# Performance work log

Hardware: AMD Instinct MI355X
Metric: run time of the kernel (lower is better)

The kernel has to match this reference:

```python
import jax, jax.numpy as jnp
import numpy as np

# Forest layout: 6 levels, children of node i at level L are contiguous at level L+1.
LEVEL_SIZES = [4096, 16384, 65536, 131072, 262144, 262144]
OFF = np.concatenate([[0], np.cumsum(LEVEL_SIZES)]).astype(np.int64)
N_NODES = int(OFF[-1])
VOCAB = 50000
D_IN = 128
HID = 128
N_CLASS = 4
W_SCALE = 0.08  # keep gate pre-activations in a sane range


def setup_inputs() -> dict:
    key = jax.random.key(0)
    ks = jax.random.split(key, 24)
    inp = {}
    inp["sen"] = jax.random.randint(ks[0], (N_NODES,), 0, VOCAB, dtype=jnp.int32)
    inp["embedding"] = jax.random.normal(ks[1], (VOCAB, D_IN), jnp.float32)
    names = ["ix", "ih", "fx", "fh", "ox", "oh", "ux", "uh"]
    for j, nm in enumerate(names):
        din = D_IN if nm.endswith("x") else HID
        inp["W_" + nm] = jax.random.normal(ks[2 + j], (din, HID), jnp.float32) * W_SCALE
        inp["b_" + nm] = jnp.zeros((HID,), jnp.float32)
    inp["W_out"] = jax.random.normal(ks[20], (HID, N_CLASS), jnp.float32) * W_SCALE
    inp["b_out"] = jnp.zeros((N_CLASS,), jnp.float32)
    return inp


def _forward(sen, embedding, W_ix, b_ix, W_ih, b_ih, W_fx, b_fx, W_fh, b_fh,
             W_ox, b_ox, W_oh, b_oh, W_ux, b_ux, W_uh, b_uh, W_out, b_out):
    emb = embedding[sen]                               # [N, D_in] gather
    h_all = jnp.zeros((N_NODES, HID), emb.dtype)
    c_all = jnp.zeros((N_NODES, HID), emb.dtype)
    L_last = len(LEVEL_SIZES) - 1
    for L in range(L_last, -1, -1):                    # bottom-up over levels
        o0, o1 = int(OFF[L]), int(OFF[L + 1])
        nL = LEVEL_SIZES[L]
        x = emb[o0:o1]                                 # [nL, D_in]
        if L == L_last:                                # leaves: no children
            h_sum = jnp.zeros((nL, HID), emb.dtype)
            fc_sum = jnp.zeros((nL, HID), emb.dtype)
        else:
            c0, c1 = int(OFF[L + 1]), int(OFF[L + 2])
            ratio = LEVEL_SIZES[L + 1] // nL           # children per node
            hc = h_all[c0:c1].reshape(nL, ratio, HID)  # children h
            cc = c_all[c0:c1].reshape(nL, ratio, HID)  # children c
            h_sum = hc.sum(axis=1)
            # per-child forget gate: sigmoid(fx(x_parent) + fh(h_child))
            f = jax.nn.sigmoid((x @ W_fx + b_fx)[:, None, :] + hc @ W_fh + b_fh)
            fc_sum = (f * cc).sum(axis=1)
        i = jax.nn.sigmoid(x @ W_ix + b_ix + h_sum @ W_ih + b_ih)
        og = jax.nn.sigmoid(x @ W_ox + b_ox + h_sum @ W_oh + b_oh)
        u = jnp.tanh(x @ W_ux + b_ux + h_sum @ W_uh + b_uh)
        c = i * u + fc_sum
        h = og * jnp.tanh(c)
        h_all = h_all.at[o0:o1].set(h)
        c_all = c_all.at[o0:o1].set(c)
    root_h = h_all[: LEVEL_SIZES[0]]                   # level-0 nodes
    return root_h @ W_out + b_out                      # [n_roots, 4] logits


def reference(sen, embedding, W_ix, b_ix, W_ih, b_ih, W_fx, b_fx, W_fh, b_fh,
              W_ox, b_ox, W_oh, b_oh, W_ux, b_ux, W_uh, b_uh, W_out, b_out):
    return _forward(sen, embedding, W_ix, b_ix, W_ih, b_ih, W_fx, b_fx, W_fh, b_fh,
                    W_ox, b_ox, W_oh, b_oh, W_ux, b_ux, W_uh, b_uh, W_out, b_out)
```

## Files before the change

### kernel.cpp

```cpp
#include <hip/hip_runtime.h>
#include <hip/hip_bf16.h>
#include <cstdio>

typedef unsigned short u16;
typedef __bf16 bf16x8 __attribute__((ext_vector_type(8)));
typedef float  floatx4 __attribute__((ext_vector_type(4)));

__device__ __forceinline__ float bf2f(u16 u) {
  union { unsigned int i; float f; } v; v.i = ((unsigned int)u) << 16; return v.f;
}
__device__ __forceinline__ u16 f2bf(float f) {
  union { float f; unsigned int i; } v; v.f = f;
  unsigned int x = v.i;
  return (u16)((x + 0x7fffu + ((x >> 16) & 1u)) >> 16);
}
__device__ __forceinline__ unsigned int f2bf_pk(float a, float b) {
  __hip_bfloat162 h = __float22bfloat162_rn(make_float2(a, b));
  union { __hip_bfloat162 h; unsigned int u; } v; v.h = h; return v.u;
}
__device__ __forceinline__ float sigmoidf_(float x) {
  return __builtin_amdgcn_rcpf(1.f + __expf(-x));
}
__device__ __forceinline__ float tanhf_(float x) {
  return fmaf(-2.f, __builtin_amdgcn_rcpf(1.f + __expf(2.f * x)), 1.f);
}

__device__ __forceinline__ int swz128(int row, int c16) {
  return row * 128 + ((c16 ^ (row & 15)) << 3);
}
__device__ __forceinline__ int swze(int row, int col) {
  return row * 128 + (((((col >> 3)) ^ (row & 15)) << 3) | (col & 7));
}

__global__ __launch_bounds__(256, 2) void proj_e(
    const float* __restrict__ emb, const u16* __restrict__ WT,
    const float* __restrict__ bsum, u16* __restrict__ Ep)
{
  __shared__ __align__(16) u16 ldsA[128 * 128];
  const int tid = threadIdx.x;
  const long m0 = (long)blockIdx.x * 128;
  {
    const int r = tid >> 1, half = tid & 1;
    long row = m0 + r; if (row > 49999) row = 49999;
    const float* src = emb + row * 128 + half * 64;
#pragma unroll
    for (int i = 0; i < 8; i++) {
      float4 v0 = *reinterpret_cast<const float4*>(src + i * 8);
      float4 v1 = *reinterpret_cast<const float4*>(src + i * 8 + 4);
      unsigned int ov[4] = { f2bf_pk(v0.x, v0.y), f2bf_pk(v0.z, v0.w),
                             f2bf_pk(v1.x, v1.y), f2bf_pk(v1.z, v1.w) };
      *reinterpret_cast<uint4*>(&ldsA[swz128(r, half * 8 + i)]) =
          *reinterpret_cast<const uint4*>(ov);
    }
  }
  __syncthreads();
  const int lane = tid & 63, w = tid >> 6, l16 = lane & 15, quad = lane >> 4;
#pragma unroll
  for (int half = 0; half < 2; half++) {
    const int col = w * 32 + half * 16 + l16;
    bf16x8 bI[4], bU[4], bO[4], bF[4];
#pragma unroll
    for (int ks = 0; ks < 4; ks++) {
      const size_t o_ = ks * 32 + quad * 8;
      bI[ks] = *reinterpret_cast<const bf16x8*>(WT + (size_t)(0   + col) * 128 + o_);
      bU[ks] = *reinterpret_cast<const bf16x8*>(WT + (size_t)(128 + col) * 128 + o_);
      bO[ks] = *reinterpret_cast<const bf16x8*>(WT + (size_t)(256 + col) * 128 + o_);
      bF[ks] = *reinterpret_cast<const bf16x8*>(WT + (size_t)(384 + col) * 128 + o_);
    }
    const float bi = bsum[col], bu = bsum[128 + col], bo = bsum[256 + col], bf = bsum[384 + col];
#pragma unroll
    for (int i = 0; i < 8; i++) {
      floatx4 aI = {0.f,0.f,0.f,0.f}, aU = {0.f,0.f,0.f,0.f};
      floatx4 aO = {0.f,0.f,0.f,0.f}, aF = {0.f,0.f,0.f,0.f};
#pragma unroll
      for (int ks = 0; ks < 4; ks++) {
        bf16x8 a = *reinterpret_cast<const bf16x8*>(&ldsA[swz128(i * 16 + l16, ks * 4 + quad)]);
        aI = __builtin_amdgcn_mfma_f32_16x16x32_bf16(a, bI[ks], aI, 0, 0, 0);
        aU = __builtin_amdgcn_mfma_f32_16x16x32_bf16(a, bU[ks], aU, 0, 0, 0);
        aO = __builtin_amdgcn_mfma_f32_16x16x32_bf16(a, bO[ks], aO, 0, 0, 0);
        aF = __builtin_amdgcn_mfma_f32_16x16x32_bf16(a, bF[ks], aF, 0, 0, 0);
      }
#pragma unroll
      for (int r2 = 0; r2 < 4; r2++) {
        const long row = m0 + i * 16 + quad * 4 + r2;
        if (row < 50000) {
          u16 ov[4] = { f2bf(aI[r2] + bi), f2bf(aU[r2] + bu),
                        f2bf(aO[r2] + bo), f2bf(aF[r2] + bf) };
          *reinterpret_cast<ushort4*>(Ep + row * 512 + col * 4) =
              *reinterpret_cast<const ushort4*>(ov);
        }
      }
    }
  }
}

__global__ void leaf_hc(const u16* __restrict__ Ep,
                        u16* __restrict__ Hl, u16* __restrict__ Cl)
{
  const int tid = threadIdx.x;
  const int r = tid >> 6, c2 = tid & 63;
  const size_t v = (size_t)blockIdx.x * 4 + r;
  uint4 g = *reinterpret_cast<const uint4*>(Ep + v * 512 + (size_t)c2 * 8);
  const u16* p = reinterpret_cast<const u16*>(&g);
  float c0 = sigmoidf_(bf2f(p[0])) * tanhf_(bf2f(p[1]));
  float c1 = sigmoidf_(bf2f(p[4])) * tanhf_(bf2f(p[5]));
  float h0 = sigmoidf_(bf2f(p[2])) * tanhf_(c0);
  float h1 = sigmoidf_(bf2f(p[6])) * tanhf_(c1);
  *reinterpret_cast<unsigned int*>(Hl + v * 128 + c2 * 2) = f2bf_pk(h0, h1);
  *reinterpret_cast<unsigned int*>(Cl + v * 128 + c2 * 2) = f2bf_pk(c0, c1);
}

__global__ __launch_bounds__(256, 2) void k_l3fused(
    const int* __restrict__ sen, const u16* __restrict__ Ep,
    const u16* __restrict__ Hl, const u16* __restrict__ Cl,
    const u16* __restrict__ BfT, const u16* __restrict__ BihT,
    const u16* __restrict__ BuhT, const u16* __restrict__ BohT,
    u16* __restrict__ c_out, u16* __restrict__ h_out,
    long o0, long o1, long o2)
{
  constexpr int PM = 32, CM = 64, NCI = 4, RT = 2;
  __shared__ __align__(16) u16 ldsH[CM * 128];
  __shared__ __align__(16) u16 ldsC[CM * 128];
  __shared__ __align__(16) u16 ldsA[CM * 128];
  __shared__ int sidC[CM];
  __shared__ int sidP[PM];

  const int tid = threadIdx.x;
  const long p0 = (long)blockIdx.x * PM;
  const long cb = (long)blockIdx.x * CM;

  {
    const int r = (tid & 127) >> 1, half = tid & 1;
    const size_t vc = (size_t)sen[o2 + cb + r];
    if (tid < 128) {
      const u16* hs = Hl + vc * 128;
#pragma unroll
      for (int ii = 0; ii < 8; ii++) {
        const int c16 = half * 8 + ii;
        *reinterpret_cast<uint4*>(&ldsH[swz128(r, c16)]) =
            *reinterpret_cast<const uint4*>(hs + c16 * 8);
      }
    } else {
      const u16* cs = Cl + vc * 128;
#pragma unroll
      for (int ii = 0; ii < 8; ii++) {
        const int c16 = half * 8 + ii;
        *reinterpret_cast<uint4*>(&ldsC[swz128(r, c16)]) =
            *reinterpret_cast<const uint4*>(cs + c16 * 8);
      }
    }
    if (tid < CM) sidC[tid] = sen[o1 + cb + tid];
    if (tid < PM) sidP[tid] = sen[o0 + p0 + tid];
  }
  __syncthreads();

  const int lane = tid & 63, w = tid >> 6, l16 = lane & 15, quad = lane >> 4;

#define LDE(I,R2) (*reinterpret_cast<const ushort4*>( \
    Ep + (size_t)sidC[(I) * 16 + quad * 4 + (R2)] * 512 + col * 4))
#define EPI1(R2, E) { \
    const int row = rbase + (R2); \
    const float iv = sigmoidf_(aI[R2] + bf2f((E).x)); \
    const float uv = tanhf_   (aU[R2] + bf2f((E).y)); \
    const float ov = sigmoidf_(aO[R2] + bf2f((E).z)); \
    const float fv = sigmoidf_(aF[R2] + bf2f((E).w)); \
    const int sl = swze(row, col); \
    const float c4 = fmaf(iv, uv, fv * bf2f(ldsC[sl])); \
    const float h4 = ov * tanhf_(c4); \
    ldsC[sl] = f2bf(c4); \
    ldsA[sl] = f2bf(h4); \
  }
#pragma unroll
  for (int gl = 0; gl < 2; gl++) {
    const int col = w * 32 + gl * 16 + l16;
    ushort4 e0 = LDE(0, 0), e1 = LDE(0, 1), e2 = LDE(0, 2), e3 = LDE(0, 3);
    bf16x8 hI[4], hU[4], hO[4], hF[4];
#pragma unroll
    for (int ks = 0; ks < 4; ks++) {
      const size_t ho = (size_t)col * 128 + ks * 32 + quad * 8;
      hI[ks] = *reinterpret_cast<const bf16x8*>(BihT + ho);
      hU[ks] = *reinterpret_cast<const bf16x8*>(BuhT + ho);
      hO[ks] = *reinterpret_cast<const bf16x8*>(BohT + ho);
      hF[ks] = *reinterpret_cast<const bf16x8*>(BfT  + ho);
    }
#pragma unroll
    for (int i = 0; i < NCI; i++) {
      ushort4 n0 = e0, n1 = e1, n2 = e2, n3 = e3;
      if (i + 1 < NCI) {
        n0 = LDE(i + 1, 0); n1 = LDE(i + 1, 1);
        n2 = LDE(i + 1, 2); n3 = LDE(i + 1, 3);
      }
      floatx4 aI = {0.f,0.f,0.f,0.f}, aU = {0.f,0.f,0.f,0.f};
      floatx4 aO = {0.f,0.f,0.f,0.f}, aF = {0.f,0.f,0.f,0.f};
#pragma unroll
      for (int ks = 0; ks < 4; ks++) {
        bf16x8 ah = *reinterpret_cast<const bf16x8*>(&ldsH[swz128(i * 16 + l16, ks * 4 + quad)]);
        aI = __builtin_amdgcn_mfma_f32_16x16x32_bf16(ah, hI[ks], aI, 0, 0, 0);
        aU = __builtin_amdgcn_mfma_f32_16x16x32_bf16(ah, hU[ks], aU, 0, 0, 0);
        aO = __builtin_amdgcn_mfma_f32_16x16x32_bf16(ah, hO[ks], aO, 0, 0, 0);
        aF = __builtin_amdgcn_mfma_f32_16x16x32_bf16(ah, hF[ks], aF, 0, 0, 0);
      }
      const int rbase = i * 16 + quad * 4;
      EPI1(0, e0) EPI1(1, e1) EPI1(2, e2) EPI1(3, e3)
      e0 = n0; e1 = n1; e2 = n2; e3 = n3;
    }
  }
#undef LDE
#undef EPI1
  __syncthreads();

#define LDG(I,T) (*reinterpret_cast<const ushort4*>( \
    Ep + (size_t)sidP[(((I) * 16 + quad * 4) >> 1) + (T)] * 512 + col * 4))
#define EPI2(T, G) { \
    const int p = (rbase >> 1) + (T); \
    const float epf = bf2f((G).w); \
    float fsum = 0.f, isum = 0.f, usum = 0.f, osum = 0.f; \
    _Pragma("unroll") \
    for (int r2 = (T) * RT; r2 < (T) * RT + RT; r2++) { \
      const int row = rbase + r2; \
      const float cch = bf2f(ldsC[swze(row, col)]); \
      fsum += sigmoidf_(aF[r2] + epf) * cch; \
      isum += aI[r2]; usum += aU[r2]; osum += aO[r2]; \
    } \
    const float c = sigmoidf_(isum + bf2f((G).x)) * tanhf_(usum + bf2f((G).y)) + fsum; \
    const float h = sigmoidf_(osum + bf2f((G).z)) * tanhf_(c); \
    c_out[(p0 + p) * 128 + col] = f2bf(c); \
    h_out[(p0 + p) * 128 + col] = f2bf(h); \
  }
#pragma unroll
  for (int gl = 0; gl < 2; gl++) {
    const int col = w * 32 + gl * 16 + l16;
    ushort4 g0 = LDG(0, 0), g1 = LDG(0, 1);
    bf16x8 bF[4], bI[4], bU[4], bO[4];
#pragma unroll
    for (int ks = 0; ks < 4; ks++) {
      const size_t bo_ = (size_t)col * 128 + ks * 32 + quad * 8;
      bF[ks] = *reinterpret_cast<const bf16x8*>(BfT + bo_);
      bI[ks] = *reinterpret_cast<const bf16x8*>(BihT + bo_);
      bU[ks] = *reinterpret_cast<const bf16x8*>(BuhT + bo_);
      bO[ks] = *reinterpret_cast<const bf16x8*>(BohT + bo_);
    }
#pragma unroll
    for (int i = 0; i < NCI; i++) {
      ushort4 m0 = g0, m1 = g1;
      if (i + 1 < NCI) { m0 = LDG(i + 1, 0); m1 = LDG(i + 1, 1); }
      floatx4 aF = {0.f,0.f,0.f,0.f}, aI = {0.f,0.f,0.f,0.f};
      floatx4 aU = {0.f,0.f,0.f,0.f}, aO = {0.f,0.f,0.f,0.f};
#pragma unroll
      for (int ks = 0; ks < 4; ks++) {
        bf16x8 a = *reinterpret_cast<const bf16x8*>(&ldsA[swz128(i * 16 + l16, ks * 4 + quad)]);
        aF = __builtin_amdgcn_mfma_f32_16x16x32_bf16(a, bF[ks], aF, 0, 0, 0);
        aI = __builtin_amdgcn_mfma_f32_16x16x32_bf16(a, bI[ks], aI, 0, 0, 0);
        aU = __builtin_amdgcn_mfma_f32_16x16x32_bf16(a, bU[ks], aU, 0, 0, 0);
        aO = __builtin_amdgcn_mfma_f32_16x16x32_bf16(a, bO[ks], aO, 0, 0, 0);
      }
      const int rbase = i * 16 + quad * 4;
      EPI2(0, g0) EPI2(1, g1)
      g0 = m0; g1 = m1;
    }
  }
#undef LDG
#undef EPI2
}

template<int LR>
__global__ __launch_bounds__(256, 2) void k_level(
    const int* __restrict__ sen, const u16* __restrict__ Ep,
    const u16* __restrict__ h_prev, const u16* __restrict__ c_prev,
    const u16* __restrict__ BfT, const u16* __restrict__ BihT,
    const u16* __restrict__ BuhT, const u16* __restrict__ BohT,
    u16* __restrict__ c_out, u16* __restrict__ h_out,
    long o0)
{
  constexpr int PM  = (LR == 2) ? 32 : 64;
  constexpr int CM  = PM << LR;
  constexpr int NCI = CM / 16;
  constexpr int RT  = 1 << LR;
  constexpr int RTI = 4 >> LR;
  constexpr int TPR = 256 / CM;
  __shared__ __align__(16) u16 ldsA[CM * 128];
  __shared__ int sidP[PM];

  const int tid = threadIdx.x;
  const long p0 = (long)blockIdx.x * PM;
  const long cb = (long)blockIdx.x * CM;

  {
    const int r = tid / TPR, q = tid % TPR;
    constexpr int CH = 16 / TPR;
    const u16* src = h_prev + (cb + r) * 128;
#pragma unroll
    for (int ii = 0; ii < CH; ii++) {
      const int c16 = q * CH + ii;
      *reinterpret_cast<uint4*>(&ldsA[swz128(r, c16)]) =
          *reinterpret_cast<const uint4*>(src + c16 * 8);
    }
    if (tid < PM) sidP[tid] = sen[o0 + p0 + tid];
  }
  __syncthreads();

  const int lane = tid & 63, w = tid >> 6, l16 = lane & 15, quad = lane >> 4;

#pragma unroll
  for (int gl = 0; gl < 2; gl++) {
    const int col = w * 32 + gl * 16 + l16;
    bf16x8 bF[4], bI[4], bU[4], bO[4];
#pragma unroll
    for (int ks = 0; ks < 4; ks++) {
      const size_t bo_ = (size_t)col * 128 + ks * 32 + quad * 8;
      bF[ks] = *reinterpret_cast<const bf16x8*>(BfT + bo_);
      bI[ks] = *reinterpret_cast<const bf16x8*>(BihT + bo_);
      bU[ks] = *reinterpret_cast<const bf16x8*>(BuhT + bo_);
      bO[ks] = *reinterpret_cast<const bf16x8*>(BohT + bo_);
    }
#pragma unroll
    for (int i = 0; i < NCI; i++) {
      const int rbase = i * 16 + quad * 4;
      ushort4 g4p[RTI];
      u16 cch16[RTI][RT];
#pragma unroll
      for (int t = 0; t < RTI; t++) {
        g4p[t] = *reinterpret_cast<const ushort4*>(
            Ep + (size_t)sidP[(rbase >> LR) + t] * 512 + col * 4);
#pragma unroll
        for (int r2 = 0; r2 < RT; r2++)
          cch16[t][r2] = c_prev[(cb + rbase + t * RT + r2) * 128 + col];
      }
      floatx4 aF = {0.f,0.f,0.f,0.f}, aI = {0.f,0.f,0.f,0.f};
      floatx4 aU = {0.f,0.f,0.f,0.f}, aO = {0.f,0.f,0.f,0.f};
#pragma unroll
      for (int ks = 0; ks < 4; ks++) {
        bf16x8 a = *reinterpret_cast<const bf16x8*>(&ldsA[swz128(i * 16 + l16, ks * 4 + quad)]);
        aF = __builtin_amdgcn_mfma_f32_16x16x32_bf16(a, bF[ks], aF, 0, 0, 0);
        aI = __builtin_amdgcn_mfma_f32_16x16x32_bf16(a, bI[ks], aI, 0, 0, 0);
        aU = __builtin_amdgcn_mfma_f32_16x16x32_bf16(a, bU[ks], aU, 0, 0, 0);
        aO = __builtin_amdgcn_mfma_f32_16x16x32_bf16(a, bO[ks], aO, 0, 0, 0);
      }
#pragma unroll
      for (int t = 0; t < RTI; t++) {
        const int p = (rbase >> LR) + t;
        const ushort4 g4 = g4p[t];
        const float epf = bf2f(g4.w);
        float fsum = 0.f, isum = 0.f, usum = 0.f, osum = 0.f;
#pragma unroll
        for (int r2 = t * RT; r2 < t * RT + RT; r2++) {
          const float cch = bf2f(cch16[t][r2 - t * RT]);
          fsum += sigmoidf_(aF[r2] + epf) * cch;
          isum += aI[r2]; usum += aU[r2]; osum += aO[r2];
        }
        const float c = sigmoidf_(isum + bf2f(g4.x)) * tanhf_(usum + bf2f(g4.y)) + fsum;
        const float h = sigmoidf_(osum + bf2f(g4.z)) * tanhf_(c);
        c_out[(p0 + p) * 128 + col] = f2bf(c);
        h_out[(p0 + p) * 128 + col] = f2bf(h);
      }
    }
  }
}

__global__ void build_wallT(const float* __restrict__ Wix, const float* __restrict__ Wux,
                            const float* __restrict__ Wox, const float* __restrict__ Wfx,
                            u16* __restrict__ WT)
{
  int idx = blockIdx.x * 256 + threadIdx.x;
  int n = idx >> 7, k = idx & 127;
  int g = n >> 7, j = n & 127;
  const float* W = (g == 0) ? Wix : (g == 1) ? Wux : (g == 2) ? Wox : Wfx;
  WT[idx] = f2bf(W[k * 128 + j]);
}

__global__ void build_bsum(const float* __restrict__ b_ix, const float* __restrict__ b_ih,
                           const float* __restrict__ b_ux, const float* __restrict__ b_uh,
                           const float* __restrict__ b_ox, const float* __restrict__ b_oh,
                           const float* __restrict__ b_fx, const float* __restrict__ b_fh,
                           float* __restrict__ bsum)
{
  int n = blockIdx.x * 256 + threadIdx.x;
  int g = n >> 7, j = n & 127;
  float v = (g == 0) ? b_ix[j] + b_ih[j] : (g == 1) ? b_ux[j] + b_uh[j]
          : (g == 2) ? b_ox[j] + b_oh[j] : b_fx[j] + b_fh[j];
  bsum[n] = v;
}

__global__ void build_bt128(const float* __restrict__ W, u16* __restrict__ BT) {
  int idx = blockIdx.x * 256 + threadIdx.x;
  int n = idx >> 7, k = idx & 127;
  BT[idx] = f2bf(W[k * 128 + n]);
}

__global__ void out_proj(const u16* __restrict__ h_root, const float* __restrict__ W_out,
                         const float* __restrict__ b_out, float* __restrict__ out)
{
  int idx = blockIdx.x * 256 + threadIdx.x;
  int n = idx >> 2, cls = idx & 3;
  float s = b_out[cls];
  for (int k = 0; k < 128; k++)
    s += bf2f(h_root[(long)n * 128 + k]) * W_out[k * 4 + cls];
  out[idx] = s;
}

extern "C" void kernel_launch(void* const* d_in, const int* in_sizes, int n_in,
                              void* d_out, int out_size, void* d_ws, size_t ws_size,
                              hipStream_t stream)
{
  const int*   sen  = (const int*)d_in[0];
  const float* emb  = (const float*)d_in[1];
  const float* W_ix = (const float*)d_in[2];  const float* b_ix = (const float*)d_in[3];
  const float* W_ih = (const float*)d_in[4];  const float* b_ih = (const float*)d_in[5];
  const float* W_fx = (const float*)d_in[6];  const float* b_fx = (const float*)d_in[7];
  const float* W_fh = (const float*)d_in[8];  const float* b_fh = (const float*)d_in[9];
  const float* W_ox = (const float*)d_in[10]; const float* b_ox = (const float*)d_in[11];
  const float* W_oh = (const float*)d_in[12]; const float* b_oh = (const float*)d_in[13];
  const float* W_ux = (const float*)d_in[14]; const float* b_ux = (const float*)d_in[15];
  const float* W_uh = (const float*)d_in[16]; const float* b_uh = (const float*)d_in[17];
  const float* W_out= (const float*)d_in[18]; const float* b_out= (const float*)d_in[19];
  float* out = (float*)d_out;

  const size_t EPB = (size_t)50000 * 512 * 2;
  const size_t TBB = (size_t)50000 * 128 * 2;
  const size_t H3  = (size_t)131072 * 128 * 2;
  const size_t H2  = (size_t)65536  * 128 * 2;
  const size_t H1  = (size_t)16384  * 128 * 2;
  const size_t H0  = (size_t)4096   * 128 * 2;
  const size_t need = EPB + 2 * TBB + 2 * (H3 + H2 + H1 + H0)
                    + (size_t)512 * 128 * 2 + 4 * (size_t)128 * 128 * 2 + 512 * 4 + 8192;
  fprintf(stderr, "[tree_lstm] ws_size=%zu need=%zu\n", ws_size, need);
  if (ws_size < need) {
    fprintf(stderr, "[tree_lstm] INSUFFICIENT WORKSPACE — skipping launch\n");
    return;
  }
  char* ws = (char*)d_ws;
  size_t off = 0;
  auto take = [&](size_t bytes) { char* p = ws + off; off += (bytes + 255) & ~(size_t)255; return p; };
  u16* Ep = (u16*)take(EPB);
  u16* Hl = (u16*)take(TBB);
  u16* Cl = (u16*)take(TBB);
  u16* h3 = (u16*)take(H3);  u16* c3 = (u16*)take(H3);
  u16* h2 = (u16*)take(H2);  u16* c2 = (u16*)take(H2);
  u16* h1 = (u16*)take(H1);  u16* c1 = (u16*)take(H1);
  u16* h0 = (u16*)take(H0);  u16* c0 = (u16*)take(H0);
  u16* WallT = (u16*)take((size_t)512 * 128 * 2);
  u16* BihT = (u16*)take((size_t)128 * 128 * 2);
  u16* BuhT = (u16*)take((size_t)128 * 128 * 2);
  u16* BohT = (u16*)take((size_t)128 * 128 * 2);
  u16* BfhT = (u16*)take((size_t)128 * 128 * 2);
  float* bsum = (float*)take(512 * 4);

  build_wallT<<<256, 256, 0, stream>>>(W_ix, W_ux, W_ox, W_fx, WallT);
  build_bsum<<<2, 256, 0, stream>>>(b_ix, b_ih, b_ux, b_uh, b_ox, b_oh, b_fx, b_fh, bsum);
  build_bt128<<<64, 256, 0, stream>>>(W_ih, BihT);
  build_bt128<<<64, 256, 0, stream>>>(W_uh, BuhT);
  build_bt128<<<64, 256, 0, stream>>>(W_oh, BohT);
  build_bt128<<<64, 256, 0, stream>>>(W_fh, BfhT);
  proj_e<<<391, 256, 0, stream>>>(emb, WallT, bsum, Ep);
  leaf_hc<<<12500, 256, 0, stream>>>(Ep, Hl, Cl);

  const long LOFF[6] = {0, 4096, 20480, 86016, 217088, 479232};

  k_l3fused<<<4096, 256, 0, stream>>>(sen, Ep, Hl, Cl,
      BfhT, BihT, BuhT, BohT, c3, h3, LOFF[3], LOFF[4], LOFF[5]);
  k_level<1><<<1024, 256, 0, stream>>>(sen, Ep, h3, c3,
      BfhT, BihT, BuhT, BohT, c2, h2, LOFF[2]);
  k_level<2><<<512, 256, 0, stream>>>(sen, Ep, h2, c2,
      BfhT, BihT, BuhT, BohT, c1, h1, LOFF[1]);
  k_level<2><<<128, 256, 0, stream>>>(sen, Ep, h1, c1,
      BfhT, BihT, BuhT, BohT, c0, h0, LOFF[0]);

  out_proj<<<64, 256, 0, stream>>>(h0, W_out, b_out, out);
}
```

Measured before the change: 483.8 us.

## Fuse leaf h/c into projection, merge prep kernels, halve l3 tile

The leaf h/c computation is folded into the embedding projection epilogue, so the separate leaf_hc kernel and its re-read of Ep go away. The six weight and bias prep kernels are merged into one launch to cut launch overhead. The fused level-3 kernel tile is halved (16 parents, 32 children per block) with twice the grid, giving more blocks and less LDS per block. The tradeoffs are scalar 2-byte H/C stores in proj_e and less reuse per block in k_l3fused.

```diff
diff --git a/kernel.cpp b/kernel.cpp
--- a/kernel.cpp
+++ b/kernel.cpp
@@ -34,7 +34,8 @@
 
 __global__ __launch_bounds__(256, 2) void proj_e(
     const float* __restrict__ emb, const u16* __restrict__ WT,
-    const float* __restrict__ bsum, u16* __restrict__ Ep)
+    const float* __restrict__ bsum, u16* __restrict__ Ep,
+    u16* __restrict__ Hl, u16* __restrict__ Cl)
 {
   __shared__ __align__(16) u16 ldsA[128 * 128];
   const int tid = threadIdx.x;
@@ -88,26 +89,14 @@
                         f2bf(aO[r2] + bo), f2bf(aF[r2] + bf) };
           *reinterpret_cast<ushort4*>(Ep + row * 512 + col * 4) =
               *reinterpret_cast<const ushort4*>(ov);
+          const float cv = sigmoidf_(bf2f(ov[0])) * tanhf_(bf2f(ov[1]));
+          const float hv = sigmoidf_(bf2f(ov[2])) * tanhf_(cv);
+          Cl[row * 128 + col] = f2bf(cv);
+          Hl[row * 128 + col] = f2bf(hv);
         }
       }
     }
   }
-}
-
-__global__ void leaf_hc(const u16* __restrict__ Ep,
-                        u16* __restrict__ Hl, u16* __restrict__ Cl)
-{
-  const int tid = threadIdx.x;
-  const int r = tid >> 6, c2 = tid & 63;
-  const size_t v = (size_t)blockIdx.x * 4 + r;
-  uint4 g = *reinterpret_cast<const uint4*>(Ep + v * 512 + (size_t)c2 * 8);
-  const u16* p = reinterpret_cast<const u16*>(&g);
-  float c0 = sigmoidf_(bf2f(p[0])) * tanhf_(bf2f(p[1]));
-  float c1 = sigmoidf_(bf2f(p[4])) * tanhf_(bf2f(p[5]));
-  float h0 = sigmoidf_(bf2f(p[2])) * tanhf_(c0);
-  float h1 = sigmoidf_(bf2f(p[6])) * tanhf_(c1);
-  *reinterpret_cast<unsigned int*>(Hl + v * 128 + c2 * 2) = f2bf_pk(h0, h1);
-  *reinterpret_cast<unsigned int*>(Cl + v * 128 + c2 * 2) = f2bf_pk(c0, c1);
 }
 
 __global__ __launch_bounds__(256, 2) void k_l3fused(
@@ -118,7 +107,7 @@
     u16* __restrict__ c_out, u16* __restrict__ h_out,
     long o0, long o1, long o2)
 {
-  constexpr int PM = 32, CM = 64, NCI = 4, RT = 2;
+  constexpr int PM = 16, CM = 32, NCI = 2, RT = 2;
   __shared__ __align__(16) u16 ldsH[CM * 128];
   __shared__ __align__(16) u16 ldsC[CM * 128];
   __shared__ __align__(16) u16 ldsA[CM * 128];
@@ -130,21 +119,21 @@
   const long cb = (long)blockIdx.x * CM;
 
   {
-    const int r = (tid & 127) >> 1, half = tid & 1;
+    const int r = (tid & 127) >> 2, q = tid & 3;
     const size_t vc = (size_t)sen[o2 + cb + r];
     if (tid < 128) {
       const u16* hs = Hl + vc * 128;
 #pragma unroll
-      for (int ii = 0; ii < 8; ii++) {
-        const int c16 = half * 8 + ii;
+      for (int ii = 0; ii < 4; ii++) {
+        const int c16 = q * 4 + ii;
         *reinterpret_cast<uint4*>(&ldsH[swz128(r, c16)]) =
             *reinterpret_cast<const uint4*>(hs + c16 * 8);
       }
     } else {
       const u16* cs = Cl + vc * 128;
 #pragma unroll
-      for (int ii = 0; ii < 8; ii++) {
-        const int c16 = half * 8 + ii;
+      for (int ii = 0; ii < 4; ii++) {
+        const int c16 = q * 4 + ii;
         *reinterpret_cast<uint4*>(&ldsC[swz128(r, c16)]) =
             *reinterpret_cast<const uint4*>(cs + c16 * 8);
       }
@@ -357,34 +346,38 @@
   }
 }
 
-__global__ void build_wallT(const float* __restrict__ Wix, const float* __restrict__ Wux,
-                            const float* __restrict__ Wox, const float* __restrict__ Wfx,
-                            u16* __restrict__ WT)
-{
-  int idx = blockIdx.x * 256 + threadIdx.x;
-  int n = idx >> 7, k = idx & 127;
-  int g = n >> 7, j = n & 127;
-  const float* W = (g == 0) ? Wix : (g == 1) ? Wux : (g == 2) ? Wox : Wfx;
-  WT[idx] = f2bf(W[k * 128 + j]);
-}
-
-__global__ void build_bsum(const float* __restrict__ b_ix, const float* __restrict__ b_ih,
-                           const float* __restrict__ b_ux, const float* __restrict__ b_uh,
-                           const float* __restrict__ b_ox, const float* __restrict__ b_oh,
-                           const float* __restrict__ b_fx, const float* __restrict__ b_fh,
-                           float* __restrict__ bsum)
-{
-  int n = blockIdx.x * 256 + threadIdx.x;
-  int g = n >> 7, j = n & 127;
-  float v = (g == 0) ? b_ix[j] + b_ih[j] : (g == 1) ? b_ux[j] + b_uh[j]
-          : (g == 2) ? b_ox[j] + b_oh[j] : b_fx[j] + b_fh[j];
-  bsum[n] = v;
-}
-
-__global__ void build_bt128(const float* __restrict__ W, u16* __restrict__ BT) {
-  int idx = blockIdx.x * 256 + threadIdx.x;
-  int n = idx >> 7, k = idx & 127;
-  BT[idx] = f2bf(W[k * 128 + n]);
+__global__ void build_prep(
+    const float* __restrict__ Wix, const float* __restrict__ Wux,
+    const float* __restrict__ Wox, const float* __restrict__ Wfx,
+    const float* __restrict__ Wih, const float* __restrict__ Wuh,
+    const float* __restrict__ Woh, const float* __restrict__ Wfh,
+    const float* __restrict__ b_ix, const float* __restrict__ b_ih,
+    const float* __restrict__ b_ux, const float* __restrict__ b_uh,
+    const float* __restrict__ b_ox, const float* __restrict__ b_oh,
+    const float* __restrict__ b_fx, const float* __restrict__ b_fh,
+    u16* __restrict__ WT, u16* __restrict__ BihT, u16* __restrict__ BuhT,
+    u16* __restrict__ BohT, u16* __restrict__ BfhT, float* __restrict__ bsum)
+{
+  const int idx = blockIdx.x * 256 + threadIdx.x;
+  if (idx < 65536) {
+    int n = idx >> 7, k = idx & 127;
+    int g = n >> 7, j = n & 127;
+    const float* W = (g == 0) ? Wix : (g == 1) ? Wux : (g == 2) ? Wox : Wfx;
+    WT[idx] = f2bf(W[k * 128 + j]);
+  } else if (idx < 131072) {
+    int t = idx - 65536;
+    int tb = t >> 14, i2 = t & 16383;
+    int n = i2 >> 7, k = i2 & 127;
+    const float* W = (tb == 0) ? Wih : (tb == 1) ? Wuh : (tb == 2) ? Woh : Wfh;
+    u16* BT = (tb == 0) ? BihT : (tb == 1) ? BuhT : (tb == 2) ? BohT : BfhT;
+    BT[i2] = f2bf(W[k * 128 + n]);
+  } else if (idx < 131584) {
+    int s = idx - 131072;
+    int g = s >> 7, j = s & 127;
+    float v = (g == 0) ? b_ix[j] + b_ih[j] : (g == 1) ? b_ux[j] + b_uh[j]
+            : (g == 2) ? b_ox[j] + b_oh[j] : b_fx[j] + b_fh[j];
+    bsum[s] = v;
+  }
 }
 
 __global__ void out_proj(const u16* __restrict__ h_root, const float* __restrict__ W_out,
@@ -445,18 +438,14 @@
   u16* BfhT = (u16*)take((size_t)128 * 128 * 2);
   float* bsum = (float*)take(512 * 4);
 
-  build_wallT<<<256, 256, 0, stream>>>(W_ix, W_ux, W_ox, W_fx, WallT);
-  build_bsum<<<2, 256, 0, stream>>>(b_ix, b_ih, b_ux, b_uh, b_ox, b_oh, b_fx, b_fh, bsum);
-  build_bt128<<<64, 256, 0, stream>>>(W_ih, BihT);
-  build_bt128<<<64, 256, 0, stream>>>(W_uh, BuhT);
-  build_bt128<<<64, 256, 0, stream>>>(W_oh, BohT);
-  build_bt128<<<64, 256, 0, stream>>>(W_fh, BfhT);
-  proj_e<<<391, 256, 0, stream>>>(emb, WallT, bsum, Ep);
-  leaf_hc<<<12500, 256, 0, stream>>>(Ep, Hl, Cl);
+  build_prep<<<514, 256, 0, stream>>>(W_ix, W_ux, W_ox, W_fx, W_ih, W_uh, W_oh, W_fh,
+      b_ix, b_ih, b_ux, b_uh, b_ox, b_oh, b_fx, b_fh,
+      WallT, BihT, BuhT, BohT, BfhT, bsum);
+  proj_e<<<391, 256, 0, stream>>>(emb, WallT, bsum, Ep, Hl, Cl);
 
   const long LOFF[6] = {0, 4096, 20480, 86016, 217088, 479232};
 
-  k_l3fused<<<4096, 256, 0, stream>>>(sen, Ep, Hl, Cl,
+  k_l3fused<<<8192, 256, 0, stream>>>(sen, Ep, Hl, Cl,
       BfhT, BihT, BuhT, BohT, c3, h3, LOFF[3], LOFF[4], LOFF[5]);
   k_level<1><<<1024, 256, 0, stream>>>(sen, Ep, h3, c3,
       BfhT, BihT, BuhT, BohT, c2, h2, LOFF[2]);
```

New measurement: 609.9 us. +26.1%, slower.
